# Kernel tuning notes

Hardware: AMD Instinct MI355X
Metric: run time of the kernel (lower is better)

## Reference

```python
import jax, jax.numpy as jnp
import numpy as np
from jax import lax

DILATION = 2


def setup_inputs() -> dict:
    key = jax.random.key(0)
    k1, k2, k3 = jax.random.split(key, 3)
    x = jax.random.normal(k1, (2048, 4096), dtype=jnp.float32)      # [T, num_inputs]
    weights = jax.random.normal(k2, (32, 16), dtype=jnp.float32)    # [num_lags, num_filters]
    biases = jax.random.normal(k3, (16,), dtype=jnp.float32) * 0.1  # [num_filters]
    return {"x": x, "weights": weights, "biases": biases}


def reference(x, weights, biases):
    T, num_inputs = x.shape
    L, F = weights.shape  # num_lags, num_filters

    # pos_constraint: clip weights at 0; normalize_weights: l2-normalize over lag axis
    w_p = jnp.maximum(weights, 0.0)
    w_pn = w_p * lax.rsqrt(jnp.maximum(jnp.sum(w_p * w_p, axis=0, keepdims=True), 1e-12))

    # reverse in time, pad num_lags zeros at the end -> causal filter of length 2L
    padded_filt = jnp.concatenate([w_pn[::-1], jnp.zeros((L, F), dtype=w_pn.dtype)], axis=0)
    kernel = padded_filt.reshape(2 * L, 1, 1, F)  # HWIO

    # [T, num_inputs] -> transpose -> [num_inputs, T, 1, 1] (NHWC, batch = input units)
    shaped_input = x.T.reshape(num_inputs, T, 1, 1)

    pre = lax.conv_general_dilated(
        shaped_input, kernel,
        window_strides=(1, 1),
        padding='SAME',
        rhs_dilation=(DILATION, 1),
        dimension_numbers=('NHWC', 'HWIO', 'NHWC'),
    )  # [num_inputs, T, 1, F]

    post = jax.nn.relu(pre + biases)  # bias broadcast over filters, relu activation

    # transpose to [T, num_inputs, 1, F] -> [T, num_inputs*F]
    out = jnp.transpose(post, (1, 0, 2, 3)).reshape(T, num_inputs * F)
    return out
```

## Files before the change

kernel.cpp:

```cpp
#include <hip/hip_runtime.h>


constexpr int T = 2048;
constexpr int N = 4096;
constexpr int L = 32;
constexpr int F = 16;
constexpr int BT = 64;
constexpr int BN = 32;
constexpr int RP = 68;
constexpr int OUT_STRIDE = N * F;

typedef float f4 __attribute__((ext_vector_type(4)));
typedef float f2 __attribute__((ext_vector_type(2)));

__global__ __launch_bounds__(256, 4)
void tlayer_kernel(const float* __restrict__ x,
                   const float* __restrict__ w,
                   const float* __restrict__ bias,
                   float* __restrict__ out)
{
    __shared__ __align__(16) float sxT[2 * BN * RP];
    __shared__ float sw[L * F];
    __shared__ float sscale[F];

    const int tid = threadIdx.x;
    const int n0  = blockIdx.x * BN;
    const int t0  = blockIdx.y * BT;

    sw[tid]       = fmaxf(w[tid], 0.f);
    sw[tid + 256] = fmaxf(w[tid + 256], 0.f);
    __syncthreads();
    if (tid < F) {
        float s = 0.f;
        #pragma unroll
        for (int l = 0; l < L; ++l) { float v = sw[l * F + tid]; s += v * v; }
        sscale[tid] = rsqrtf(fmaxf(s, 1e-12f));
    }
    __syncthreads();
    sw[tid]       *= sscale[tid & 15];
    sw[tid + 256] *= sscale[tid & 15];

    for (int idx = tid; idx < 126 * (BN / 4); idx += 256) {
        const int r  = idx >> 3;
        const int c4 = idx & 7;
        const int g  = t0 - 63 + r;
        f4 v = {0.f, 0.f, 0.f, 0.f};
        if (g >= 0 && g < T)
            v = *(const f4*)(x + (size_t)g * N + n0 + c4 * 4);
        const int p  = r & 1;
        const int rr = r >> 1;
        float* dst = sxT + p * (BN * RP) + (c4 * 4) * RP + rr;
        dst[0 * RP] = v[0];
        dst[1 * RP] = v[1];
        dst[2 * RP] = v[2];
        dst[3 * RP] = v[3];
    }
    __syncthreads();

    const int fp = tid & 7;
    const int nl = tid >> 3;
    const f2 b2 = *(const f2*)(bias + fp * 2);

    f2 wr[L];
    #pragma unroll
    for (int l = 0; l < L; ++l)
        wr[l] = *(const f2*)(sw + l * F + fp * 2);

    const float* myrow = sxT + nl * RP;
    float* outbase = out + (size_t)(n0 + nl) * F + fp * 2;

    #pragma unroll 1
    for (int grp = 0; grp < 16; ++grp) {
        const int toff = (grp & 1) + (grp >> 1) * 8;
        const int p    = grp & 1;
        const int r0p  = (grp >> 1) * 4;
        const float* src = myrow + p * (BN * RP) + r0p;

        f2 acc[4] = {b2, b2, b2, b2};

        f4 xa[5];
        #pragma unroll
        for (int u = 0; u < 5; ++u)
            xa[u] = *(const f4*)(src + 4 * u);

        #pragma unroll
        for (int l = 16; l < 32; ++l) {
            const f2 wl = wr[l];
            #pragma unroll
            for (int j = 0; j < 4; ++j) {
                const int m = 31 + j - l;
                acc[j] += wl * xa[m >> 2][m & 3];
            }
        }

        f4 xb[5];
        #pragma unroll
        for (int u = 0; u < 5; ++u)
            xb[u] = *(const f4*)(src + 16 + 4 * u);

        #pragma unroll
        for (int l = 0; l < 16; ++l) {
            const f2 wl = wr[l];
            #pragma unroll
            for (int j = 0; j < 4; ++j) {
                const int k = 15 + j - l;
                acc[j] += wl * xb[k >> 2][k & 3];
            }
        }

        #pragma unroll
        for (int j = 0; j < 4; ++j) {
            f2 r;
            r[0] = fmaxf(acc[j][0], 0.f);
            r[1] = fmaxf(acc[j][1], 0.f);
            *(f2*)(outbase + (size_t)(t0 + toff + 2 * j) * OUT_STRIDE) = r;
        }
    }
}

extern "C" void kernel_launch(void* const* d_in, const int* in_sizes, int n_in,
                              void* d_out, int out_size, void* d_ws, size_t ws_size,
                              hipStream_t stream) {
    const float* x    = (const float*)d_in[0];
    const float* w    = (const float*)d_in[1];
    const float* bias = (const float*)d_in[2];
    float* out = (float*)d_out;

    dim3 grid(N / BN, T / BT);
    tlayer_kernel<<<grid, 256, 0, stream>>>(x, w, bias, out);
}
```

Measured before the change: 549.1 us.

## Restructure conv tiling so each block computes two time rows across all inputs

Each block now handles a pair of output time steps (t0 and t0+2) that share 32 of their 33 input rows, and sweeps all 4096 input units in 128-wide chunks. The next chunk is prefetched from global memory into registers and then written to a double-buffered shared tile while the current chunk is computed. Output writes become contiguous full rows, which should suit the write-bound output. The cost is that each input row is re-read by roughly 16 blocks, where the old time-tiled layout used about 2 reads. There are also fewer blocks (1024) and the occupancy hint is lower.

Result: slower. 616.4 us (+12.3%).

```diff
diff --git a/kernel.cpp b/kernel.cpp
--- a/kernel.cpp
+++ b/kernel.cpp
@@ -5,27 +5,28 @@
 constexpr int N = 4096;
 constexpr int L = 32;
 constexpr int F = 16;
-constexpr int BT = 64;
-constexpr int BN = 32;
-constexpr int RP = 68;
+constexpr int NC = 128;
+constexpr int NCHUNK = N / NC;
+constexpr int NR = 33;
 constexpr int OUT_STRIDE = N * F;
 
 typedef float f4 __attribute__((ext_vector_type(4)));
 typedef float f2 __attribute__((ext_vector_type(2)));
 
-__global__ __launch_bounds__(256, 4)
+__global__ __launch_bounds__(256, 2)
 void tlayer_kernel(const float* __restrict__ x,
                    const float* __restrict__ w,
                    const float* __restrict__ bias,
                    float* __restrict__ out)
 {
-    __shared__ __align__(16) float sxT[2 * BN * RP];
+    __shared__ __align__(16) float xs[2][NR * NC];
     __shared__ float sw[L * F];
     __shared__ float sscale[F];
 
     const int tid = threadIdx.x;
-    const int n0  = blockIdx.x * BN;
-    const int t0  = blockIdx.y * BT;
+    const int b   = blockIdx.x;
+    const int t0  = (b & 1) + (b >> 1) * 4;
+    const int tb  = t0 + 2;
 
     sw[tid]       = fmaxf(w[tid], 0.f);
     sw[tid + 256] = fmaxf(w[tid + 256], 0.f);
@@ -39,82 +40,101 @@
     __syncthreads();
     sw[tid]       *= sscale[tid & 15];
     sw[tid + 256] *= sscale[tid & 15];
-
-    for (int idx = tid; idx < 126 * (BN / 4); idx += 256) {
-        const int r  = idx >> 3;
-        const int c4 = idx & 7;
-        const int g  = t0 - 63 + r;
-        f4 v = {0.f, 0.f, 0.f, 0.f};
-        if (g >= 0 && g < T)
-            v = *(const f4*)(x + (size_t)g * N + n0 + c4 * 4);
-        const int p  = r & 1;
-        const int rr = r >> 1;
-        float* dst = sxT + p * (BN * RP) + (c4 * 4) * RP + rr;
-        dst[0 * RP] = v[0];
-        dst[1 * RP] = v[1];
-        dst[2 * RP] = v[2];
-        dst[3 * RP] = v[3];
-    }
     __syncthreads();
 
     const int fp = tid & 7;
-    const int nl = tid >> 3;
-    const f2 b2 = *(const f2*)(bias + fp * 2);
+    const int ng = tid >> 3;
 
     f2 wr[L];
     #pragma unroll
     for (int l = 0; l < L; ++l)
         wr[l] = *(const f2*)(sw + l * F + fp * 2);
+    const f2 b2 = *(const f2*)(bias + fp * 2);
 
-    const float* myrow = sxT + nl * RP;
-    float* outbase = out + (size_t)(n0 + nl) * F + fp * 2;
+
+    {
+        #pragma unroll
+        for (int u = 0; u < 4; ++u) {
+            const int idx = tid + u * 256;
+            const int r = idx >> 5, c4 = idx & 31;
+            const int g = tb - 1 - 2 * r;
+            f4 v = {0.f, 0.f, 0.f, 0.f};
+            if (g >= 0) v = *(const f4*)(x + (size_t)g * N + c4 * 4);
+            *(f4*)(&xs[0][r * NC + c4 * 4]) = v;
+        }
+        if (tid < 32) {
+            const int g = tb - 65;
+            f4 v = {0.f, 0.f, 0.f, 0.f};
+            if (g >= 0) v = *(const f4*)(x + (size_t)g * N + tid * 4);
+            *(f4*)(&xs[0][32 * NC + tid * 4]) = v;
+        }
+    }
+    __syncthreads();
+
+    float* orowA = out + (size_t)t0 * OUT_STRIDE;
+    float* orowB = out + (size_t)tb * OUT_STRIDE;
 
     #pragma unroll 1
-    for (int grp = 0; grp < 16; ++grp) {
-        const int toff = (grp & 1) + (grp >> 1) * 8;
-        const int p    = grp & 1;
-        const int r0p  = (grp >> 1) * 4;
-        const float* src = myrow + p * (BN * RP) + r0p;
+    for (int c = 0; c < NCHUNK; ++c) {
+        const int cur = c & 1;
 
-        f2 acc[4] = {b2, b2, b2, b2};
-
-        f4 xa[5];
-        #pragma unroll
-        for (int u = 0; u < 5; ++u)
-            xa[u] = *(const f4*)(src + 4 * u);
-
-        #pragma unroll
-        for (int l = 16; l < 32; ++l) {
-            const f2 wl = wr[l];
+        f4 ld[5];
+        if (c + 1 < NCHUNK) {
+            const int cn1 = (c + 1) * NC;
             #pragma unroll
-            for (int j = 0; j < 4; ++j) {
-                const int m = 31 + j - l;
-                acc[j] += wl * xa[m >> 2][m & 3];
+            for (int u = 0; u < 4; ++u) {
+                const int idx = tid + u * 256;
+                const int r = idx >> 5, c4 = idx & 31;
+                const int g = tb - 1 - 2 * r;
+                ld[u] = {0.f, 0.f, 0.f, 0.f};
+                if (g >= 0) ld[u] = *(const f4*)(x + (size_t)g * N + cn1 + c4 * 4);
+            }
+            ld[4] = {0.f, 0.f, 0.f, 0.f};
+            if (tid < 32) {
+                const int g = tb - 65;
+                if (g >= 0) ld[4] = *(const f4*)(x + (size_t)g * N + cn1 + tid * 4);
             }
         }
 
-        f4 xb[5];
+        const float* xb = &xs[cur][4 * ng];
+        f2 aA[4] = {b2, b2, b2, b2};
+        f2 aB[4] = {b2, b2, b2, b2};
         #pragma unroll
-        for (int u = 0; u < 5; ++u)
-            xb[u] = *(const f4*)(src + 16 + 4 * u);
-
-        #pragma unroll
-        for (int l = 0; l < 16; ++l) {
-            const f2 wl = wr[l];
-            #pragma unroll
-            for (int j = 0; j < 4; ++j) {
-                const int k = 15 + j - l;
-                acc[j] += wl * xb[k >> 2][k & 3];
+        for (int r = 0; r < NR; ++r) {
+            const f4 xv = *(const f4*)(xb + r * NC);
+            if (r < L) {
+                const f2 wl = wr[r];
+                aB[0] += wl * xv[0]; aB[1] += wl * xv[1];
+                aB[2] += wl * xv[2]; aB[3] += wl * xv[3];
+            }
+            if (r >= 1) {
+                const f2 wl = wr[r - 1];
+                aA[0] += wl * xv[0]; aA[1] += wl * xv[1];
+                aA[2] += wl * xv[2]; aA[3] += wl * xv[3];
             }
         }
 
+        const int nbase = c * NC + 4 * ng;
         #pragma unroll
-        for (int j = 0; j < 4; ++j) {
-            f2 r;
-            r[0] = fmaxf(acc[j][0], 0.f);
-            r[1] = fmaxf(acc[j][1], 0.f);
-            *(f2*)(outbase + (size_t)(t0 + toff + 2 * j) * OUT_STRIDE) = r;
+        for (int k = 0; k < 4; ++k) {
+            f2 rA, rB;
+            rA[0] = fmaxf(aA[k][0], 0.f); rA[1] = fmaxf(aA[k][1], 0.f);
+            rB[0] = fmaxf(aB[k][0], 0.f); rB[1] = fmaxf(aB[k][1], 0.f);
+            *(f2*)(orowA + (size_t)(nbase + k) * F + fp * 2) = rA;
+            *(f2*)(orowB + (size_t)(nbase + k) * F + fp * 2) = rB;
         }
+
+        if (c + 1 < NCHUNK) {
+            #pragma unroll
+            for (int u = 0; u < 4; ++u) {
+                const int idx = tid + u * 256;
+                const int r = idx >> 5, c4 = idx & 31;
+                *(f4*)(&xs[cur ^ 1][r * NC + c4 * 4]) = ld[u];
+            }
+            if (tid < 32)
+                *(f4*)(&xs[cur ^ 1][32 * NC + tid * 4]) = ld[4];
+        }
+        __syncthreads();
     }
 }
 
@@ -126,6 +146,6 @@
     const float* bias = (const float*)d_in[2];
     float* out = (float*)d_out;
 
-    dim3 grid(N / BN, T / BT);
+    dim3 grid(T / 2);
     tlayer_kernel<<<grid, 256, 0, stream>>>(x, w, bias, out);
 }
```
